# Optimization experiments

Measured on AMD Instinct MI355X. Metric: run time of the kernel, lower is better.

## Reference

```python
import jax, jax.numpy as jnp
import numpy as np

B, T, E, H = 8, 2048, 1024, 128

def setup_inputs() -> dict:
    key = jax.random.key(0)
    k1, k2, k3, k4 = jax.random.split(key, 4)
    s = 0.02
    return {
        "x":  jax.random.normal(k1, (B, T, E), dtype=jnp.float32),
        "Wq": jax.random.normal(k2, (E, H), dtype=jnp.float32) * s,
        "Wk": jax.random.normal(k3, (E, H), dtype=jnp.float32) * s,
        "Wv": jax.random.normal(k4, (E, H), dtype=jnp.float32) * s,
    }

def reference(x, Wq, Wk, Wv):
    # q,k,v: [B,T,H]
    q = jnp.einsum("bte,eh->bth", x, Wq)
    k = jnp.einsum("bte,eh->bth", x, Wk)
    v = jnp.einsum("bte,eh->bth", x, Wv)
    scale = jnp.asarray(q.shape[-1], q.dtype) ** -0.5
    wei = jnp.einsum("bqh,bkh->bqk", q, k) * scale  # [B,T,T]
    causal = jnp.tril(jnp.ones((wei.shape[1], wei.shape[2]), dtype=bool))
    wei = jnp.where(causal, wei, jnp.asarray(-jnp.inf, wei.dtype))
    wei = jax.nn.softmax(wei, axis=-1)
    # dropout_prob = 0.0 -> identity
    return jnp.einsum("bqk,bkh->bqh", wei, v)
```

## Files before the change

### kernel.cpp

```cpp
#include <hip/hip_runtime.h>

#define BB 8
#define TT 2048
#define EE 1024
#define HH 128

typedef __bf16 bf16;
typedef __attribute__((ext_vector_type(8))) __bf16 bf16x8;
typedef __attribute__((ext_vector_type(4))) __bf16 bf16x4;
typedef __attribute__((ext_vector_type(4))) float f32x4;

__device__ __host__ inline int qb_off(int qb) {
  int h = qb >> 1;
  return qb + h * (h - 1) + ((qb & 1) ? h : 0);
}
#define NSLAB 72

__device__ inline void gload_lds16(const bf16* g, bf16* l) {
  __builtin_amdgcn_global_load_lds((const __attribute__((address_space(1))) unsigned int*)g,
                                   (__attribute__((address_space(3))) unsigned int*)l,
                                   16, 0, 0);
}

__global__ __launch_bounds__(256) void wt_kernel(const float* __restrict__ wq,
                                                 const float* __restrict__ wk,
                                                 const float* __restrict__ wv,
                                                 bf16* __restrict__ wt) {
  __shared__ float tile[64][65];
  const int z = blockIdx.z;
  const float* w = (z == 0) ? wq : ((z == 1) ? wk : wv);
  const int k0 = blockIdx.x * 64;
  const int h0 = blockIdx.y * 64;
  const int c = threadIdx.x & 63;
  const int r0 = threadIdx.x >> 6;
#pragma unroll
  for (int i = 0; i < 16; ++i) {
    int tt = r0 + i * 4;
    tile[tt][c] = w[(size_t)(k0 + tt) * HH + h0 + c];
  }
  __syncthreads();
#pragma unroll
  for (int i = 0; i < 16; ++i) {
    int hh = r0 + i * 4;
    wt[((size_t)(z * HH + h0 + hh)) * EE + k0 + c] = (bf16)tile[c][hh];
  }
}

__global__ __launch_bounds__(256) void xcvt_kernel(const float* __restrict__ x,
                                                   bf16* __restrict__ xb) {
  const size_t base = (size_t)blockIdx.x * 4096 + threadIdx.x * 4;
#pragma unroll
  for (int j = 0; j < 4; ++j) {
    size_t idx = base + j * 1024;
    f32x4 xv = *(const f32x4*)(x + idx);
    bf16x4 xo;
#pragma unroll
    for (int i = 0; i < 4; ++i) xo[i] = (bf16)xv[i];
    *(bf16x4*)(xb + idx) = xo;
  }
}

__global__ __launch_bounds__(256) void gemm_kernel(const bf16* __restrict__ xb,
                                                   const bf16* __restrict__ wt,
                                                   bf16* __restrict__ q,
                                                   bf16* __restrict__ k,
                                                   bf16* __restrict__ v) {
  __shared__ bf16 As[128 * 32];
  __shared__ bf16 Bs[96 * 32];
  const int tid = threadIdx.x;
  const int lane = tid & 63;
  const int wave = tid >> 6;
  const int l16 = lane & 15;
  const int quad = lane >> 4;
  const int wm = wave & 1;
  const int wn = wave >> 1;
  const int bm = blockIdx.x;
  const int ntile = blockIdx.y;

  const int trow = tid >> 2;
  const int tsub = (tid & 3) * 8;
  const bf16* gA = xb + (size_t)(bm * 128 + trow) * EE + tsub;
  const bf16* gB = wt + (size_t)(ntile * 96 + trow) * EE + tsub;

  f32x4 acc[4][3];
#pragma unroll
  for (int rg = 0; rg < 4; ++rg)
#pragma unroll
    for (int nt = 0; nt < 3; ++nt) acc[rg][nt] = f32x4{0.f, 0.f, 0.f, 0.f};

  for (int ks = 0; ks < EE / 32; ++ks) {
    gload_lds16(gA + ks * 32, &As[wave * 512]);
    gload_lds16(gA + (size_t)64 * EE + ks * 32, &As[2048 + wave * 512]);
    gload_lds16(gB + ks * 32, &Bs[wave * 512]);
    if (tid < 128)
      gload_lds16(gB + (size_t)64 * EE + ks * 32, &Bs[2048 + wave * 512]);
    __syncthreads();

    bf16x8 af[4], bf[3];
#pragma unroll
    for (int rg = 0; rg < 4; ++rg)
      af[rg] = *(const bf16x8*)&As[(wm * 64 + rg * 16 + l16) * 32 + quad * 8];
#pragma unroll
    for (int nt = 0; nt < 3; ++nt)
      bf[nt] = *(const bf16x8*)&Bs[(wn * 48 + nt * 16 + l16) * 32 + quad * 8];
#pragma unroll
    for (int rg = 0; rg < 4; ++rg)
#pragma unroll
      for (int nt = 0; nt < 3; ++nt)
        acc[rg][nt] = __builtin_amdgcn_mfma_f32_16x16x32_bf16(af[rg], bf[nt], acc[rg][nt], 0, 0, 0);
    __syncthreads();
  }

  bf16* outp[3] = {q, k, v};
#pragma unroll
  for (int rg = 0; rg < 4; ++rg)
#pragma unroll
    for (int nt = 0; nt < 3; ++nt) {
      int col = ntile * 96 + wn * 48 + nt * 16 + l16;
      int z = col >> 7;
      int n = col & 127;
#pragma unroll
      for (int r = 0; r < 4; ++r) {
        int row = bm * 128 + wm * 64 + rg * 16 + quad * 4 + r;
        outp[z][(size_t)row * HH + n] = (bf16)acc[rg][nt][r];
      }
    }
}

__global__ __launch_bounds__(256) void vtrans_kernel(const bf16* __restrict__ v,
                                                     bf16* __restrict__ vt) {
  __shared__ bf16 tile[64][65];
  const int b = blockIdx.x;
  const int t0 = blockIdx.y * 64;
  const int h0 = blockIdx.z * 64;
  const int c = threadIdx.x & 63;
  const int r0 = threadIdx.x >> 6;
#pragma unroll
  for (int i = 0; i < 16; ++i) {
    int tt = r0 + i * 4;
    tile[tt][c] = v[((size_t)(b * TT + t0 + tt)) * HH + h0 + c];
  }
  __syncthreads();
#pragma unroll
  for (int i = 0; i < 16; ++i) {
    int hh = r0 + i * 4;
    vt[((size_t)(b * HH + h0 + hh)) * TT + t0 + c] = tile[c][hh];
  }
}

__global__ __launch_bounds__(256, 2) void flash_kernel(const bf16* __restrict__ q,
                                                       const bf16* __restrict__ k,
                                                       const bf16* __restrict__ vt,
                                                       bf16* __restrict__ opart,
                                                       float* __restrict__ lpart) {
  const int b = blockIdx.x & 7;
  int j = blockIdx.x >> 3;
  int qb = 0, ns = 1;
  while (j >= ns) { j -= ns; ++qb; ns = ((2 * qb + 1) >> 2) + 1; }
  const int s = j;
  const int kt0 = s * 4;
  const int kt1 = min(kt0 + 3, 2 * qb + 1);

  const int lane = threadIdx.x & 63;
  const int wave = threadIdx.x >> 6;
  const int l16 = lane & 15;
  const int quad = lane >> 4;
  const int wrow0 = qb * 128 + wave * 32;

  __shared__ float pbuf[4][32 * 68];
  float* pb = &pbuf[wave][0];

  bf16x8 qf[2][4];
#pragma unroll
  for (int rg = 0; rg < 2; ++rg) {
    const bf16* qbp = q + (size_t)(b * TT + wrow0 + rg * 16 + l16) * HH + quad * 8;
#pragma unroll
    for (int ks = 0; ks < 4; ++ks) qf[rg][ks] = *(const bf16x8*)(qbp + ks * 32);
  }

  f32x4 O[2][8];
#pragma unroll
  for (int rg = 0; rg < 2; ++rg)
#pragma unroll
    for (int nt = 0; nt < 8; ++nt) O[rg][nt] = f32x4{0.f, 0.f, 0.f, 0.f};
  f32x4 O9[2] = {f32x4{0.f, 0.f, 0.f, 0.f}, f32x4{0.f, 0.f, 0.f, 0.f}};

  bf16x8 ones;
  {
    bf16 ov = (l16 == 0) ? (bf16)1.0f : (bf16)0.0f;
#pragma unroll
    for (int j2 = 0; j2 < 8; ++j2) ones[j2] = ov;
  }

  const float c_ = 0.12753257680406733f;

  for (int kt = kt0; kt <= kt1; ++kt) {
    f32x4 S[2][4];
#pragma unroll
    for (int rg = 0; rg < 2; ++rg)
#pragma unroll
      for (int nt = 0; nt < 4; ++nt) S[rg][nt] = f32x4{0.f, 0.f, 0.f, 0.f};
    const bf16* kb = k + (size_t)(b * TT + kt * 64 + l16) * HH + quad * 8;
#pragma unroll
    for (int nt = 0; nt < 4; ++nt) {
      bf16x8 kf[4];
#pragma unroll
      for (int ks = 0; ks < 4; ++ks)
        kf[ks] = *(const bf16x8*)(kb + (size_t)nt * 16 * HH + ks * 32);
#pragma unroll
      for (int ks = 0; ks < 4; ++ks) {
        S[0][nt] = __builtin_amdgcn_mfma_f32_16x16x32_bf16(qf[0][ks], kf[ks], S[0][nt], 0, 0, 0);
        S[1][nt] = __builtin_amdgcn_mfma_f32_16x16x32_bf16(qf[1][ks], kf[ks], S[1][nt], 0, 0, 0);
      }
    }

    const bf16* vb = vt + (size_t)(b * HH + l16) * TT + kt * 64 + quad * 8;
    bf16x8 vf0[8];
#pragma unroll
    for (int nt = 0; nt < 8; ++nt)
      vf0[nt] = *(const bf16x8*)(vb + (size_t)nt * 16 * TT);

#pragma unroll
    for (int rg = 0; rg < 2; ++rg)
#pragma unroll
      for (int nt = 0; nt < 4; ++nt) {
        int col = kt * 64 + nt * 16 + l16;
#pragma unroll
        for (int r = 0; r < 4; ++r) {
          int row = wrow0 + rg * 16 + quad * 4 + r;
          float p = (col <= row) ? exp2f(S[rg][nt][r] * c_) : 0.f;
          pb[(rg * 16 + quad * 4 + r) * 68 + nt * 16 + l16] = p;
        }
      }
    __asm__ volatile("s_waitcnt lgkmcnt(0)" ::: "memory");

    {
      bf16x8 af[2];
#pragma unroll
      for (int rg = 0; rg < 2; ++rg) {
        const float* pr = &pb[(rg * 16 + l16) * 68 + quad * 8];
        f32x4 a0 = *(const f32x4*)pr;
        f32x4 a1 = *(const f32x4*)(pr + 4);
#pragma unroll
        for (int j2 = 0; j2 < 4; ++j2) { af[rg][j2] = (bf16)a0[j2]; af[rg][j2 + 4] = (bf16)a1[j2]; }
      }
#pragma unroll
      for (int nt = 0; nt < 8; ++nt) {
        O[0][nt] = __builtin_amdgcn_mfma_f32_16x16x32_bf16(af[0], vf0[nt], O[0][nt], 0, 0, 0);
        O[1][nt] = __builtin_amdgcn_mfma_f32_16x16x32_bf16(af[1], vf0[nt], O[1][nt], 0, 0, 0);
      }
      O9[0] = __builtin_amdgcn_mfma_f32_16x16x32_bf16(af[0], ones, O9[0], 0, 0, 0);
      O9[1] = __builtin_amdgcn_mfma_f32_16x16x32_bf16(af[1], ones, O9[1], 0, 0, 0);
    }
    {
      bf16x8 af[2];
#pragma unroll
      for (int rg = 0; rg < 2; ++rg) {
        const float* pr = &pb[(rg * 16 + l16) * 68 + 32 + quad * 8];
        f32x4 a0 = *(const f32x4*)pr;
        f32x4 a1 = *(const f32x4*)(pr + 4);
#pragma unroll
        for (int j2 = 0; j2 < 4; ++j2) { af[rg][j2] = (bf16)a0[j2]; af[rg][j2 + 4] = (bf16)a1[j2]; }
      }
#pragma unroll
      for (int nt = 0; nt < 8; ++nt) {
        bf16x8 vf = *(const bf16x8*)(vb + (size_t)nt * 16 * TT + 32);
        O[0][nt] = __builtin_amdgcn_mfma_f32_16x16x32_bf16(af[0], vf, O[0][nt], 0, 0, 0);
        O[1][nt] = __builtin_amdgcn_mfma_f32_16x16x32_bf16(af[1], vf, O[1][nt], 0, 0, 0);
      }
      O9[0] = __builtin_amdgcn_mfma_f32_16x16x32_bf16(af[0], ones, O9[0], 0, 0, 0);
      O9[1] = __builtin_amdgcn_mfma_f32_16x16x32_bf16(af[1], ones, O9[1], 0, 0, 0);
    }
    __asm__ volatile("s_waitcnt lgkmcnt(0)" ::: "memory");
  }

  const size_t slab = (size_t)(b * NSLAB + qb_off(qb) + s);
  bf16* op = opart + slab * (128 * 128);
#pragma unroll
  for (int rg = 0; rg < 2; ++rg)
#pragma unroll
    for (int nt = 0; nt < 8; ++nt)
#pragma unroll
      for (int r = 0; r < 4; ++r) {
        int row = wave * 32 + rg * 16 + quad * 4 + r;
        op[row * 128 + nt * 16 + l16] = (bf16)O[rg][nt][r];
      }
  if (l16 == 0) {
#pragma unroll
    for (int rg = 0; rg < 2; ++rg)
#pragma unroll
      for (int r = 0; r < 4; ++r)
        lpart[slab * 128 + wave * 32 + rg * 16 + quad * 4 + r] = O9[rg][r];
  }
}

__global__ __launch_bounds__(128) void combine_kernel(const bf16* __restrict__ opart,
                                                      const float* __restrict__ lpart,
                                                      float* __restrict__ out) {
  const int b = blockIdx.x;
  const int qt16 = blockIdx.y;
  const int half = blockIdx.z;
  const int row = threadIdx.x >> 3;
  const int colo = (threadIdx.x & 7) * 8 + half * 64;
  const int qb = qt16 >> 3;
  const int srow = (qt16 & 7) * 16 + row;
  const int ns = ((2 * qb + 1) >> 2) + 1;
  const size_t slab0 = (size_t)(b * NSLAB + qb_off(qb));

  float acc[8];
#pragma unroll
  for (int j = 0; j < 8; ++j) acc[j] = 0.f;
  float L = 0.f;

  int s = 0;
  for (; s + 4 <= ns; s += 4) {
    float l0 = lpart[(slab0 + s + 0) * 128 + srow];
    float l1 = lpart[(slab0 + s + 1) * 128 + srow];
    float l2 = lpart[(slab0 + s + 2) * 128 + srow];
    float l3 = lpart[(slab0 + s + 3) * 128 + srow];
    bf16x8 v0 = *(const bf16x8*)(opart + (slab0 + s + 0) * (128 * 128) + srow * 128 + colo);
    bf16x8 v1 = *(const bf16x8*)(opart + (slab0 + s + 1) * (128 * 128) + srow * 128 + colo);
    bf16x8 v2 = *(const bf16x8*)(opart + (slab0 + s + 2) * (128 * 128) + srow * 128 + colo);
    bf16x8 v3 = *(const bf16x8*)(opart + (slab0 + s + 3) * (128 * 128) + srow * 128 + colo);
    L += (l0 + l1) + (l2 + l3);
#pragma unroll
    for (int j = 0; j < 8; ++j)
      acc[j] += ((float)v0[j] + (float)v1[j]) + ((float)v2[j] + (float)v3[j]);
  }
  for (; s < ns; ++s) {
    L += lpart[(slab0 + s) * 128 + srow];
    bf16x8 ov = *(const bf16x8*)(opart + (slab0 + s) * (128 * 128) + srow * 128 + colo);
#pragma unroll
    for (int j = 0; j < 8; ++j) acc[j] += (float)ov[j];
  }
  float invL = 1.f / L;
  float* o = out + ((size_t)(b * TT + qt16 * 16 + row)) * HH + colo;
  f32x4 o0, o1;
#pragma unroll
  for (int j = 0; j < 4; ++j) { o0[j] = acc[j] * invL; o1[j] = acc[j + 4] * invL; }
  *(f32x4*)o = o0;
  *(f32x4*)(o + 4) = o1;
}

extern "C" void kernel_launch(void* const* d_in, const int* in_sizes, int n_in,
                              void* d_out, int out_size, void* d_ws, size_t ws_size,
                              hipStream_t stream) {
  const float* x = (const float*)d_in[0];
  const float* wq = (const float*)d_in[1];
  const float* wk = (const float*)d_in[2];
  const float* wv = (const float*)d_in[3];
  float* out = (float*)d_out;

  char* ws = (char*)d_ws;
  const size_t NE = (size_t)BB * TT * HH;
  bf16* wt = (bf16*)ws;
  bf16* xb = (bf16*)(ws + (1 << 20));
  bf16* q = (bf16*)(ws + (33 << 20));
  bf16* k = q + NE;
  bf16* v = k + NE;
  bf16* vt = v + NE;
  bf16* opart = xb;
  float* lpart = (float*)(opart + (size_t)(BB * NSLAB) * 128 * 128);

  wt_kernel<<<dim3(16, 2, 3), 256, 0, stream>>>(wq, wk, wv, wt);
  xcvt_kernel<<<dim3(4096), 256, 0, stream>>>(x, xb);
  gemm_kernel<<<dim3(128, 4), 256, 0, stream>>>(xb, wt, q, k, v);
  vtrans_kernel<<<dim3(8, 32, 2), 256, 0, stream>>>(v, vt);
  flash_kernel<<<dim3(576), 256, 0, stream>>>(q, k, vt, opart, lpart);
  combine_kernel<<<dim3(8, 128, 2), 128, 0, stream>>>(opart, lpart, out);
}
```

Measured before the change: 186.4 us.

## Rewrite flash kernel with 32x32 MFMA, register-resident P, and causal skipping

Restructures the split-K flash attention kernel to compute S transposed with 32x32x16 bf16 MFMA, keep P in registers by packing to bf16 and using v_permlane32_swap instead of an LDS round-trip, and accumulate the row sum with scalar adds instead of an extra ones-matrix MFMA. Each wave now stops at its own diagonal 32-key tile, so fully masked tiles are skipped. K fragments are double-buffered across iterations and block order is reversed so the heaviest slabs launch first. MFMA sections are wrapped in s_setprio hints. The price is more register pressure from the f32x16 accumulators and prefetch buffers, plus dependence on a gfx950-specific permlane instruction.

New measurement: 186.3 us. About the same (-0.0%).

```diff
diff --git a/kernel.cpp b/kernel.cpp
--- a/kernel.cpp
+++ b/kernel.cpp
@@ -9,6 +9,7 @@
 typedef __attribute__((ext_vector_type(8))) __bf16 bf16x8;
 typedef __attribute__((ext_vector_type(4))) __bf16 bf16x4;
 typedef __attribute__((ext_vector_type(4))) float f32x4;
+typedef __attribute__((ext_vector_type(16))) float f32x16;
 
 __device__ __host__ inline int qb_off(int qb) {
   int h = qb >> 1;
@@ -148,13 +149,93 @@
   }
 }
 
+
+__device__ __forceinline__ unsigned pk2(float a, float b) {
+  union { __bf16 h[2]; unsigned u; } x;
+  x.h[0] = (__bf16)a;
+  x.h[1] = (__bf16)b;
+  return x.u;
+}
+
+__device__ __forceinline__ void plswap(unsigned& a, unsigned& b) {
+  asm volatile("v_permlane32_swap_b32 %0, %1" : "+v"(a), "+v"(b));
+}
+
+__device__ __forceinline__ void fbody(const bf16* __restrict__ kp0,
+                                      const bf16* __restrict__ vp0,
+                                      const bf16x8 (&qf)[8],
+                                      bf16x8 (&kf)[8], bf16x8 (&kfn)[8],
+                                      f32x16 (&O)[4], float& L,
+                                      int k32, int k32n, int kdiag,
+                                      int qrow, int hi) {
+  const float c_ = 0.12753257680406733f;
+  bf16x8 vf[2][4];
+#pragma unroll
+  for (int s16 = 0; s16 < 2; ++s16)
+#pragma unroll
+    for (int ht = 0; ht < 4; ++ht)
+      vf[s16][ht] = *(const bf16x8*)(vp0 + (size_t)ht * 32 * TT + k32 * 32 + s16 * 16);
+
+  f32x16 S;
+#pragma unroll
+  for (int r = 0; r < 16; ++r) S[r] = 0.f;
+  __builtin_amdgcn_s_setprio(1);
+#pragma unroll
+  for (int h16 = 0; h16 < 8; ++h16)
+    S = __builtin_amdgcn_mfma_f32_32x32x16_bf16(kf[h16], qf[h16], S, 0, 0, 0);
+  __builtin_amdgcn_s_setprio(0);
+
+#pragma unroll
+  for (int h16 = 0; h16 < 8; ++h16)
+    kfn[h16] = *(const bf16x8*)(kp0 + (size_t)k32n * 32 * HH + h16 * 16);
+
+  float p[16];
+  if (k32 == kdiag) {
+    const int kkb = k32 * 32 + 4 * hi;
+#pragma unroll
+    for (int r = 0; r < 16; ++r) {
+      int kk = kkb + (r & 3) + 8 * (r >> 2);
+      float pv = (kk <= qrow) ? exp2f(S[r] * c_) : 0.f;
+      p[r] = pv;
+      L += pv;
+    }
+  } else {
+#pragma unroll
+    for (int r = 0; r < 16; ++r) {
+      float pv = exp2f(S[r] * c_);
+      p[r] = pv;
+      L += pv;
+    }
+  }
+
+#pragma unroll
+  for (int s16 = 0; s16 < 2; ++s16) {
+    unsigned w0 = pk2(p[s16 * 8 + 0], p[s16 * 8 + 1]);
+    unsigned w1 = pk2(p[s16 * 8 + 2], p[s16 * 8 + 3]);
+    unsigned w2 = pk2(p[s16 * 8 + 4], p[s16 * 8 + 5]);
+    unsigned w3 = pk2(p[s16 * 8 + 6], p[s16 * 8 + 7]);
+    plswap(w0, w2);
+    plswap(w1, w3);
+    union { unsigned u[4]; bf16x8 v; } af;
+    af.u[0] = w0;
+    af.u[1] = w1;
+    af.u[2] = w2;
+    af.u[3] = w3;
+    __builtin_amdgcn_s_setprio(1);
+#pragma unroll
+    for (int ht = 0; ht < 4; ++ht)
+      O[ht] = __builtin_amdgcn_mfma_f32_32x32x16_bf16(af.v, vf[s16][ht], O[ht], 0, 0, 0);
+    __builtin_amdgcn_s_setprio(0);
+  }
+}
+
 __global__ __launch_bounds__(256, 2) void flash_kernel(const bf16* __restrict__ q,
                                                        const bf16* __restrict__ k,
                                                        const bf16* __restrict__ vt,
                                                        bf16* __restrict__ opart,
                                                        float* __restrict__ lpart) {
   const int b = blockIdx.x & 7;
-  int j = blockIdx.x >> 3;
+  int j = (NSLAB - 1) - (blockIdx.x >> 3);
   int qb = 0, ns = 1;
   while (j >= ns) { j -= ns; ++qb; ns = ((2 * qb + 1) >> 2) + 1; }
   const int s = j;
@@ -163,135 +244,55 @@
 
   const int lane = threadIdx.x & 63;
   const int wave = threadIdx.x >> 6;
-  const int l16 = lane & 15;
-  const int quad = lane >> 4;
+  const int l32 = lane & 31;
+  const int hi = lane >> 5;
   const int wrow0 = qb * 128 + wave * 32;
-
-  __shared__ float pbuf[4][32 * 68];
-  float* pb = &pbuf[wave][0];
-
-  bf16x8 qf[2][4];
-#pragma unroll
-  for (int rg = 0; rg < 2; ++rg) {
-    const bf16* qbp = q + (size_t)(b * TT + wrow0 + rg * 16 + l16) * HH + quad * 8;
-#pragma unroll
-    for (int ks = 0; ks < 4; ++ks) qf[rg][ks] = *(const bf16x8*)(qbp + ks * 32);
-  }
-
-  f32x4 O[2][8];
-#pragma unroll
-  for (int rg = 0; rg < 2; ++rg)
-#pragma unroll
-    for (int nt = 0; nt < 8; ++nt) O[rg][nt] = f32x4{0.f, 0.f, 0.f, 0.f};
-  f32x4 O9[2] = {f32x4{0.f, 0.f, 0.f, 0.f}, f32x4{0.f, 0.f, 0.f, 0.f}};
-
-  bf16x8 ones;
+  const int qrow = wrow0 + l32;
+
+  bf16x8 qf[8];
   {
-    bf16 ov = (l16 == 0) ? (bf16)1.0f : (bf16)0.0f;
-#pragma unroll
-    for (int j2 = 0; j2 < 8; ++j2) ones[j2] = ov;
-  }
-
-  const float c_ = 0.12753257680406733f;
-
-  for (int kt = kt0; kt <= kt1; ++kt) {
-    f32x4 S[2][4];
-#pragma unroll
-    for (int rg = 0; rg < 2; ++rg)
-#pragma unroll
-      for (int nt = 0; nt < 4; ++nt) S[rg][nt] = f32x4{0.f, 0.f, 0.f, 0.f};
-    const bf16* kb = k + (size_t)(b * TT + kt * 64 + l16) * HH + quad * 8;
-#pragma unroll
-    for (int nt = 0; nt < 4; ++nt) {
-      bf16x8 kf[4];
-#pragma unroll
-      for (int ks = 0; ks < 4; ++ks)
-        kf[ks] = *(const bf16x8*)(kb + (size_t)nt * 16 * HH + ks * 32);
-#pragma unroll
-      for (int ks = 0; ks < 4; ++ks) {
-        S[0][nt] = __builtin_amdgcn_mfma_f32_16x16x32_bf16(qf[0][ks], kf[ks], S[0][nt], 0, 0, 0);
-        S[1][nt] = __builtin_amdgcn_mfma_f32_16x16x32_bf16(qf[1][ks], kf[ks], S[1][nt], 0, 0, 0);
-      }
+    const bf16* qp = q + (size_t)(b * TT + qrow) * HH + hi * 8;
+#pragma unroll
+    for (int h16 = 0; h16 < 8; ++h16) qf[h16] = *(const bf16x8*)(qp + h16 * 16);
+  }
+
+  f32x16 O[4];
+#pragma unroll
+  for (int ht = 0; ht < 4; ++ht)
+#pragma unroll
+    for (int r = 0; r < 16; ++r) O[ht][r] = 0.f;
+  float L = 0.f;
+
+  const int kdiag = qb * 4 + wave;
+  const int k32b = kt0 * 2;
+  const int k32e = min(kt1 * 2 + 1, kdiag);
+
+  const bf16* kp0 = k + ((size_t)b * TT + l32) * HH + hi * 8;
+  const bf16* vp0 = vt + ((size_t)b * HH + l32) * TT + hi * 8;
+
+  bf16x8 kfA[8], kfB[8];
+#pragma unroll
+  for (int h16 = 0; h16 < 8; ++h16)
+    kfA[h16] = *(const bf16x8*)(kp0 + (size_t)k32b * 32 * HH + h16 * 16);
+
+  for (int k32 = k32b; k32 <= k32e; k32 += 2) {
+    fbody(kp0, vp0, qf, kfA, kfB, O, L, k32, min(k32 + 1, k32e), kdiag, qrow, hi);
+    if (k32 + 1 <= k32e)
+      fbody(kp0, vp0, qf, kfB, kfA, O, L, k32 + 1, min(k32 + 2, k32e), kdiag, qrow, hi);
+  }
+
+  L += __shfl_xor(L, 32, 64);
+
+  const size_t slab = (size_t)(b * NSLAB + qb_off(qb) + s);
+  bf16* op = opart + slab * (128 * 128) + (size_t)wave * 32 * 128;
+#pragma unroll
+  for (int ht = 0; ht < 4; ++ht)
+#pragma unroll
+    for (int r = 0; r < 16; ++r) {
+      int qr = (r & 3) + 8 * (r >> 2) + 4 * hi;
+      op[qr * 128 + ht * 32 + l32] = (bf16)O[ht][r];
     }
-
-    const bf16* vb = vt + (size_t)(b * HH + l16) * TT + kt * 64 + quad * 8;
-    bf16x8 vf0[8];
-#pragma unroll
-    for (int nt = 0; nt < 8; ++nt)
-      vf0[nt] = *(const bf16x8*)(vb + (size_t)nt * 16 * TT);
-
-#pragma unroll
-    for (int rg = 0; rg < 2; ++rg)
-#pragma unroll
-      for (int nt = 0; nt < 4; ++nt) {
-        int col = kt * 64 + nt * 16 + l16;
-#pragma unroll
-        for (int r = 0; r < 4; ++r) {
-          int row = wrow0 + rg * 16 + quad * 4 + r;
-          float p = (col <= row) ? exp2f(S[rg][nt][r] * c_) : 0.f;
-          pb[(rg * 16 + quad * 4 + r) * 68 + nt * 16 + l16] = p;
-        }
-      }
-    __asm__ volatile("s_waitcnt lgkmcnt(0)" ::: "memory");
-
-    {
-      bf16x8 af[2];
-#pragma unroll
-      for (int rg = 0; rg < 2; ++rg) {
-        const float* pr = &pb[(rg * 16 + l16) * 68 + quad * 8];
-        f32x4 a0 = *(const f32x4*)pr;
-        f32x4 a1 = *(const f32x4*)(pr + 4);
-#pragma unroll
-        for (int j2 = 0; j2 < 4; ++j2) { af[rg][j2] = (bf16)a0[j2]; af[rg][j2 + 4] = (bf16)a1[j2]; }
-      }
-#pragma unroll
-      for (int nt = 0; nt < 8; ++nt) {
-        O[0][nt] = __builtin_amdgcn_mfma_f32_16x16x32_bf16(af[0], vf0[nt], O[0][nt], 0, 0, 0);
-        O[1][nt] = __builtin_amdgcn_mfma_f32_16x16x32_bf16(af[1], vf0[nt], O[1][nt], 0, 0, 0);
-      }
-      O9[0] = __builtin_amdgcn_mfma_f32_16x16x32_bf16(af[0], ones, O9[0], 0, 0, 0);
-      O9[1] = __builtin_amdgcn_mfma_f32_16x16x32_bf16(af[1], ones, O9[1], 0, 0, 0);
-    }
-    {
-      bf16x8 af[2];
-#pragma unroll
-      for (int rg = 0; rg < 2; ++rg) {
-        const float* pr = &pb[(rg * 16 + l16) * 68 + 32 + quad * 8];
-        f32x4 a0 = *(const f32x4*)pr;
-        f32x4 a1 = *(const f32x4*)(pr + 4);
-#pragma unroll
-        for (int j2 = 0; j2 < 4; ++j2) { af[rg][j2] = (bf16)a0[j2]; af[rg][j2 + 4] = (bf16)a1[j2]; }
-      }
-#pragma unroll
-      for (int nt = 0; nt < 8; ++nt) {
-        bf16x8 vf = *(const bf16x8*)(vb + (size_t)nt * 16 * TT + 32);
-        O[0][nt] = __builtin_amdgcn_mfma_f32_16x16x32_bf16(af[0], vf, O[0][nt], 0, 0, 0);
-        O[1][nt] = __builtin_amdgcn_mfma_f32_16x16x32_bf16(af[1], vf, O[1][nt], 0, 0, 0);
-      }
-      O9[0] = __builtin_amdgcn_mfma_f32_16x16x32_bf16(af[0], ones, O9[0], 0, 0, 0);
-      O9[1] = __builtin_amdgcn_mfma_f32_16x16x32_bf16(af[1], ones, O9[1], 0, 0, 0);
-    }
-    __asm__ volatile("s_waitcnt lgkmcnt(0)" ::: "memory");
-  }
-
-  const size_t slab = (size_t)(b * NSLAB + qb_off(qb) + s);
-  bf16* op = opart + slab * (128 * 128);
-#pragma unroll
-  for (int rg = 0; rg < 2; ++rg)
-#pragma unroll
-    for (int nt = 0; nt < 8; ++nt)
-#pragma unroll
-      for (int r = 0; r < 4; ++r) {
-        int row = wave * 32 + rg * 16 + quad * 4 + r;
-        op[row * 128 + nt * 16 + l16] = (bf16)O[rg][nt][r];
-      }
-  if (l16 == 0) {
-#pragma unroll
-    for (int rg = 0; rg < 2; ++rg)
-#pragma unroll
-      for (int r = 0; r < 4; ++r)
-        lpart[slab * 128 + wave * 32 + rg * 16 + quad * 4 + r] = O9[rg][r];
-  }
+  if (hi == 0) lpart[slab * 128 + wave * 32 + l32] = L;
 }
 
 __global__ __launch_bounds__(128) void combine_kernel(const bf16* __restrict__ opart,
```
